# Kernel optimization log

Hardware: AMD Instinct MI355X
Metric: run time of the kernel (lower is better)

The kernel has to match this reference:

```python
import jax, jax.numpy as jnp
import numpy as np

N1, N2, D = 8192, 8192, 128

def setup_inputs() -> dict:
    key = jax.random.key(0)
    k1, k2, k3, k4 = jax.random.split(key, 4)
    X1 = jax.random.normal(k1, (N1, D), dtype=jnp.float32)
    X2 = jax.random.normal(k2, (N2, D), dtype=jnp.float32)
    task1 = jax.random.randint(k3, (N1,), 0, 2, dtype=jnp.int32)
    task2 = jax.random.randint(k4, (N2,), 0, 2, dtype=jnp.int32)
    # learned parameters (init values match module defaults: lengthscale=1, output_variance=1, b=0)
    log_l = jnp.zeros((D,), dtype=jnp.float32)          # log(1)
    log_theta_l = jnp.zeros((1,), dtype=jnp.float32)    # log(1)
    b = jnp.zeros((1,), dtype=jnp.float32)
    return {"X1": X1, "X2": X2, "log_l": log_l, "log_theta_l": log_theta_l,
            "b": b, "task1": task1, "task2": task2}

def reference(X1, X2, log_l, log_theta_l, b, task1, task2):
    l = jnp.exp(log_l)                      # (D,) ARD lengthscales
    A = X1 / l                              # (N1, D)
    B = X2 / l                              # (N2, D)
    # sum((a-b)^2) = |a|^2 + |b|^2 - 2 a.b  -> GEMM form, no (N1,N2,D) intermediate
    sq_dist = (jnp.sum(A * A, axis=1)[:, None]
               + jnp.sum(B * B, axis=1)[None, :]
               - 2.0 * (A @ B.T))
    sq_dist = jnp.maximum(sq_dist, 0.0)
    K_base = jnp.exp(log_theta_l[0]) * jnp.exp(-0.5 * sq_dist)   # (N1, N2)
    # lambda = clip(2/(1+exp(b)) - 1, 0, 1)
    lam = jnp.clip(2.0 / (1.0 + jnp.exp(b[0])) - 1.0, 0.0, 1.0)
    diff_task = task1[:, None] != task2[None, :]                 # (N1, N2) bool
    K = K_base * jnp.where(diff_task, lam, 1.0)
    return K
```

## Files before the change

kernel.cpp:

```cpp
#include <hip/hip_runtime.h>
#include <stdint.h>

typedef float f32x4 __attribute__((ext_vector_type(4)));
typedef int   i32x4 __attribute__((ext_vector_type(4)));
typedef __bf16 bf16x8 __attribute__((ext_vector_type(8)));

#define NN 8192
#define DDIM 128
#define RSTRIDE 80

#define OFF_AH 0
#define OFF_AL 10240
#define OFF_BH 20480
#define OFF_BL 30720
#define OFF_ILS 40960
#define OFF_N1  41472
#define OFF_N2  41984
#define LDS_TOT 42496

__device__ __forceinline__ uint32_t pk2(__bf16 a, __bf16 b) {
    return (uint32_t)__builtin_bit_cast(unsigned short, a)
         | ((uint32_t)__builtin_bit_cast(unsigned short, b) << 16);
}

__device__ __forceinline__ void split4(f32x4 x, uint2& hi, uint2& lo) {
    __bf16 h0 = (__bf16)x[0], h1 = (__bf16)x[1], h2 = (__bf16)x[2], h3 = (__bf16)x[3];
    hi.x = pk2(h0, h1); hi.y = pk2(h2, h3);
    __bf16 l0 = (__bf16)(x[0] - (float)h0);
    __bf16 l1 = (__bf16)(x[1] - (float)h1);
    __bf16 l2 = (__bf16)(x[2] - (float)h2);
    __bf16 l3 = (__bf16)(x[3] - (float)h3);
    lo.x = pk2(l0, l1); lo.y = pk2(l2, l3);
}

__device__ __forceinline__ void lds_barrier() {
    asm volatile("s_waitcnt lgkmcnt(0)" ::: "memory");
    __builtin_amdgcn_sched_barrier(0);
    __builtin_amdgcn_s_barrier();
    __builtin_amdgcn_sched_barrier(0);
}

__global__ __launch_bounds__(256, 3) void tgp_kernel(
    const float* __restrict__ X1, const float* __restrict__ X2,
    const float* __restrict__ log_l,
    const float* __restrict__ log_theta_l, const float* __restrict__ bparam,
    const int* __restrict__ task1, const int* __restrict__ task2,
    float* __restrict__ C)
{
    __shared__ __align__(16) char smem[LDS_TOT];
    float* const ils = (float*)(smem + OFF_ILS);
    float* const n1s = (float*)(smem + OFF_N1);
    float* const n2s = (float*)(smem + OFF_N2);

    const int t = threadIdx.x;
    const int lane = t & 63;
    const int wv = t >> 6;
    const int wr = wv >> 1, wc = wv & 1;
    const int lr = lane & 15, lg = lane >> 4;
    const int kq = t & 7;
    const int rg = t >> 3;

    int wg = blockIdx.x;
    int xcd = wg & 7;
    int r = wg >> 3;
    int su = r >> 6;
    int inner = r & 63;
    int tm = xcd * 8 + (inner >> 3);
    int tn = su * 8 + (inner & 7);

    const float* Ag = X1 + (size_t)tm * 128 * DDIM;
    const float* Bg = X2 + (size_t)tn * 128 * DDIM;

    if (t < 128) ils[t] = __expf(-log_l[t]);

    f32x4 aV[4], bV[4];
    #pragma unroll
    for (int e = 0; e < 4; ++e) {
        aV[e] = *(const f32x4*)(Ag + (size_t)(e * 32 + rg) * DDIM + kq * 4);
        bV[e] = *(const f32x4*)(Bg + (size_t)(e * 32 + rg) * DDIM + kq * 4);
    }
    __syncthreads();

    float nA[4] = {0.f, 0.f, 0.f, 0.f};
    float nB[4] = {0.f, 0.f, 0.f, 0.f};
    f32x4 acc[4][4];
    #pragma unroll
    for (int i = 0; i < 4; ++i)
        #pragma unroll
        for (int j = 0; j < 4; ++j) acc[i][j] = (f32x4){0.f, 0.f, 0.f, 0.f};

    for (int c = 0; c < 4; ++c) {
        f32x4 il4 = *(const f32x4*)(ils + c * 32 + kq * 4);
        #pragma unroll
        for (int e = 0; e < 4; ++e) {
            int rr = e * 32 + rg;
            f32x4 xa = aV[e] * il4;
            f32x4 xb = bV[e] * il4;
            nA[e] += xa[0]*xa[0] + xa[1]*xa[1] + xa[2]*xa[2] + xa[3]*xa[3];
            nB[e] += xb[0]*xb[0] + xb[1]*xb[1] + xb[2]*xb[2] + xb[3]*xb[3];
            uint2 hA, lA, hB, lB;
            split4(xa, hA, lA);
            split4(xb, hB, lB);
            int boff = rr * RSTRIDE + kq * 8;
            *(uint2*)(smem + OFF_AH + boff) = hA;
            *(uint2*)(smem + OFF_AL + boff) = lA;
            *(uint2*)(smem + OFF_BH + boff) = hB;
            *(uint2*)(smem + OFF_BL + boff) = lB;
        }
        if (c < 3) {
            #pragma unroll
            for (int e = 0; e < 4; ++e) {
                aV[e] = *(const f32x4*)(Ag + (size_t)(e * 32 + rg) * DDIM + (c + 1) * 32 + kq * 4);
                bV[e] = *(const f32x4*)(Bg + (size_t)(e * 32 + rg) * DDIM + (c + 1) * 32 + kq * 4);
            }
        }
        lds_barrier();

        {
            bf16x8 ah[4], bh[4], xf[4];
            #pragma unroll
            for (int mi = 0; mi < 4; ++mi) {
                int off = (wr * 64 + mi * 16 + lr) * RSTRIDE + lg * 16;
                ah[mi] = *(const bf16x8*)(smem + OFF_AH + off);
            }
            #pragma unroll
            for (int ni = 0; ni < 4; ++ni) {
                int off = (wc * 64 + ni * 16 + lr) * RSTRIDE + lg * 16;
                bh[ni] = *(const bf16x8*)(smem + OFF_BH + off);
            }
            #pragma unroll
            for (int mi = 0; mi < 4; ++mi)
                #pragma unroll
                for (int ni = 0; ni < 4; ++ni)
                    acc[mi][ni] = __builtin_amdgcn_mfma_f32_16x16x32_bf16(bh[ni], ah[mi], acc[mi][ni], 0, 0, 0);
            #pragma unroll
            for (int mi = 0; mi < 4; ++mi) {
                int off = (wr * 64 + mi * 16 + lr) * RSTRIDE + lg * 16;
                xf[mi] = *(const bf16x8*)(smem + OFF_AL + off);
            }
            #pragma unroll
            for (int mi = 0; mi < 4; ++mi)
                #pragma unroll
                for (int ni = 0; ni < 4; ++ni)
                    acc[mi][ni] = __builtin_amdgcn_mfma_f32_16x16x32_bf16(bh[ni], xf[mi], acc[mi][ni], 0, 0, 0);
            #pragma unroll
            for (int ni = 0; ni < 4; ++ni) {
                int off = (wc * 64 + ni * 16 + lr) * RSTRIDE + lg * 16;
                xf[ni] = *(const bf16x8*)(smem + OFF_BL + off);
            }
            #pragma unroll
            for (int mi = 0; mi < 4; ++mi)
                #pragma unroll
                for (int ni = 0; ni < 4; ++ni)
                    acc[mi][ni] = __builtin_amdgcn_mfma_f32_16x16x32_bf16(xf[ni], ah[mi], acc[mi][ni], 0, 0, 0);
        }
        lds_barrier();
    }

    #pragma unroll
    for (int e = 0; e < 4; ++e) {
        #pragma unroll
        for (int off = 1; off < 8; off <<= 1) {
            nA[e] += __shfl_xor(nA[e], off);
            nB[e] += __shfl_xor(nB[e], off);
        }
    }
    if ((t & 7) == 0) {
        #pragma unroll
        for (int e = 0; e < 4; ++e) {
            n1s[e * 32 + rg] = nA[e];
            n2s[e * 32 + rg] = nB[e];
        }
    }
    __syncthreads();

    float logt = log_theta_l[0];
    float bb = bparam[0];
    float lam = fminf(fmaxf(2.f / (1.f + __expf(bb)) - 1.f, 0.f), 1.f);
    int rbase = tm * 128, cbase = tn * 128;

    #pragma unroll
    for (int mi = 0; mi < 4; ++mi) {
        int rowl = wr * 64 + mi * 16 + lr;
        float n1v = n1s[rowl];
        int t1v = task1[rbase + rowl];
        #pragma unroll
        for (int ni = 0; ni < 4; ++ni) {
            int coll = wc * 64 + ni * 16 + lg * 4;
            f32x4 n2v = *(const f32x4*)(n2s + coll);
            i32x4 t2v = *(const i32x4*)(task2 + cbase + coll);
            f32x4 kv;
            #pragma unroll
            for (int rix = 0; rix < 4; ++rix) {
                float s = fmaxf(n1v + n2v[rix] - 2.f * acc[mi][ni][rix], 0.f);
                float k = __expf(fmaf(-0.5f, s, logt));
                kv[rix] = (t1v != t2v[rix]) ? k * lam : k;
            }
            *(f32x4*)(C + (size_t)(rbase + rowl) * NN + cbase + coll) = kv;
        }
    }
}

extern "C" void kernel_launch(void* const* d_in, const int* in_sizes, int n_in,
                              void* d_out, int out_size, void* d_ws, size_t ws_size,
                              hipStream_t stream)
{
    const float* X1 = (const float*)d_in[0];
    const float* X2 = (const float*)d_in[1];
    const float* log_l = (const float*)d_in[2];
    const float* log_theta = (const float*)d_in[3];
    const float* bp = (const float*)d_in[4];
    const int* t1 = (const int*)d_in[5];
    const int* t2 = (const int*)d_in[6];
    float* C = (float*)d_out;
    (void)d_ws; (void)ws_size; (void)in_sizes; (void)n_in; (void)out_size;

    tgp_kernel<<<4096, 256, 0, stream>>>(X1, X2, log_l, log_theta, bp, t1, t2, C);
}
```

Baseline: 98.62 us.

## Use 512-thread blocks with 64-wide K chunks and an 8-wave output split

The block grows from 4 to 8 waves. Each wave now computes a 64x32 sub-tile instead of 64x64. The K dimension is staged in two 64-wide chunks rather than four 32-wide chunks, with a larger LDS row stride, so there are fewer barriers and the trailing barrier is gone. The register prefetch of the next chunk is removed, so global loads are no longer overlapped with MFMA work. LDS per block roughly doubles, which may limit how many blocks fit on a CU, in exchange for more waves per block to hide the latency of the output stores.

```diff
diff --git a/kernel.cpp b/kernel.cpp
--- a/kernel.cpp
+++ b/kernel.cpp
@@ -7,16 +7,16 @@
 
 #define NN 8192
 #define DDIM 128
-#define RSTRIDE 80
+#define RSTRIDE 144
 
 #define OFF_AH 0
-#define OFF_AL 10240
-#define OFF_BH 20480
-#define OFF_BL 30720
-#define OFF_ILS 40960
-#define OFF_N1  41472
-#define OFF_N2  41984
-#define LDS_TOT 42496
+#define OFF_AL 18432
+#define OFF_BH 36864
+#define OFF_BL 55296
+#define OFF_ILS 73728
+#define OFF_N1  74240
+#define OFF_N2  74752
+#define LDS_TOT 75264
 
 __device__ __forceinline__ uint32_t pk2(__bf16 a, __bf16 b) {
     return (uint32_t)__builtin_bit_cast(unsigned short, a)
@@ -40,7 +40,7 @@
     __builtin_amdgcn_sched_barrier(0);
 }
 
-__global__ __launch_bounds__(256, 3) void tgp_kernel(
+__global__ __launch_bounds__(512, 4) void tgp_kernel(
     const float* __restrict__ X1, const float* __restrict__ X2,
     const float* __restrict__ log_l,
     const float* __restrict__ log_theta_l, const float* __restrict__ bparam,
@@ -55,10 +55,10 @@
     const int t = threadIdx.x;
     const int lane = t & 63;
     const int wv = t >> 6;
-    const int wr = wv >> 1, wc = wv & 1;
+    const int wr = wv >> 2, wc = wv & 3;
     const int lr = lane & 15, lg = lane >> 4;
-    const int kq = t & 7;
-    const int rg = t >> 3;
+    const int kq = t & 15;
+    const int rg = t >> 4;
 
     int wg = blockIdx.x;
     int xcd = wg & 7;
@@ -72,100 +72,92 @@
     const float* Bg = X2 + (size_t)tn * 128 * DDIM;
 
     if (t < 128) ils[t] = __expf(-log_l[t]);
-
-    f32x4 aV[4], bV[4];
-    #pragma unroll
-    for (int e = 0; e < 4; ++e) {
-        aV[e] = *(const f32x4*)(Ag + (size_t)(e * 32 + rg) * DDIM + kq * 4);
-        bV[e] = *(const f32x4*)(Bg + (size_t)(e * 32 + rg) * DDIM + kq * 4);
-    }
     __syncthreads();
 
     float nA[4] = {0.f, 0.f, 0.f, 0.f};
     float nB[4] = {0.f, 0.f, 0.f, 0.f};
-    f32x4 acc[4][4];
+    f32x4 acc[4][2];
     #pragma unroll
     for (int i = 0; i < 4; ++i)
         #pragma unroll
-        for (int j = 0; j < 4; ++j) acc[i][j] = (f32x4){0.f, 0.f, 0.f, 0.f};
-
-    for (int c = 0; c < 4; ++c) {
-        f32x4 il4 = *(const f32x4*)(ils + c * 32 + kq * 4);
-        #pragma unroll
-        for (int e = 0; e < 4; ++e) {
-            int rr = e * 32 + rg;
-            f32x4 xa = aV[e] * il4;
-            f32x4 xb = bV[e] * il4;
-            nA[e] += xa[0]*xa[0] + xa[1]*xa[1] + xa[2]*xa[2] + xa[3]*xa[3];
-            nB[e] += xb[0]*xb[0] + xb[1]*xb[1] + xb[2]*xb[2] + xb[3]*xb[3];
-            uint2 hA, lA, hB, lB;
-            split4(xa, hA, lA);
-            split4(xb, hB, lB);
-            int boff = rr * RSTRIDE + kq * 8;
-            *(uint2*)(smem + OFF_AH + boff) = hA;
-            *(uint2*)(smem + OFF_AL + boff) = lA;
-            *(uint2*)(smem + OFF_BH + boff) = hB;
-            *(uint2*)(smem + OFF_BL + boff) = lB;
-        }
-        if (c < 3) {
+        for (int j = 0; j < 2; ++j) acc[i][j] = (f32x4){0.f, 0.f, 0.f, 0.f};
+
+    #pragma unroll
+    for (int c = 0; c < 2; ++c) {
+        {
+            f32x4 il4 = *(const f32x4*)(ils + c * 64 + kq * 4);
             #pragma unroll
             for (int e = 0; e < 4; ++e) {
-                aV[e] = *(const f32x4*)(Ag + (size_t)(e * 32 + rg) * DDIM + (c + 1) * 32 + kq * 4);
-                bV[e] = *(const f32x4*)(Bg + (size_t)(e * 32 + rg) * DDIM + (c + 1) * 32 + kq * 4);
+                int row = e * 32 + rg;
+                f32x4 xa = *(const f32x4*)(Ag + (size_t)row * DDIM + c * 64 + kq * 4);
+                f32x4 xb = *(const f32x4*)(Bg + (size_t)row * DDIM + c * 64 + kq * 4);
+                xa *= il4; xb *= il4;
+                nA[e] += xa[0]*xa[0] + xa[1]*xa[1] + xa[2]*xa[2] + xa[3]*xa[3];
+                nB[e] += xb[0]*xb[0] + xb[1]*xb[1] + xb[2]*xb[2] + xb[3]*xb[3];
+                uint2 hA, lA, hB, lB;
+                split4(xa, hA, lA);
+                split4(xb, hB, lB);
+                int boff = row * RSTRIDE + kq * 8;
+                *(uint2*)(smem + OFF_AH + boff) = hA;
+                *(uint2*)(smem + OFF_AL + boff) = lA;
+                *(uint2*)(smem + OFF_BH + boff) = hB;
+                *(uint2*)(smem + OFF_BL + boff) = lB;
             }
         }
         lds_barrier();
 
-        {
-            bf16x8 ah[4], bh[4], xf[4];
+        #pragma unroll
+        for (int ks = 0; ks < 2; ++ks) {
+            int kb = ks * 64;
+            bf16x8 ah[4], bx[2], xf[4];
             #pragma unroll
             for (int mi = 0; mi < 4; ++mi) {
-                int off = (wr * 64 + mi * 16 + lr) * RSTRIDE + lg * 16;
+                int off = (wr * 64 + mi * 16 + lr) * RSTRIDE + kb + lg * 16;
                 ah[mi] = *(const bf16x8*)(smem + OFF_AH + off);
             }
             #pragma unroll
-            for (int ni = 0; ni < 4; ++ni) {
-                int off = (wc * 64 + ni * 16 + lr) * RSTRIDE + lg * 16;
-                bh[ni] = *(const bf16x8*)(smem + OFF_BH + off);
+            for (int ni = 0; ni < 2; ++ni) {
+                int off = (wc * 32 + ni * 16 + lr) * RSTRIDE + kb + lg * 16;
+                bx[ni] = *(const bf16x8*)(smem + OFF_BH + off);
             }
             #pragma unroll
             for (int mi = 0; mi < 4; ++mi)
                 #pragma unroll
-                for (int ni = 0; ni < 4; ++ni)
-                    acc[mi][ni] = __builtin_amdgcn_mfma_f32_16x16x32_bf16(bh[ni], ah[mi], acc[mi][ni], 0, 0, 0);
+                for (int ni = 0; ni < 2; ++ni)
+                    acc[mi][ni] = __builtin_amdgcn_mfma_f32_16x16x32_bf16(bx[ni], ah[mi], acc[mi][ni], 0, 0, 0);
             #pragma unroll
             for (int mi = 0; mi < 4; ++mi) {
-                int off = (wr * 64 + mi * 16 + lr) * RSTRIDE + lg * 16;
+                int off = (wr * 64 + mi * 16 + lr) * RSTRIDE + kb + lg * 16;
                 xf[mi] = *(const bf16x8*)(smem + OFF_AL + off);
             }
             #pragma unroll
             for (int mi = 0; mi < 4; ++mi)
                 #pragma unroll
-                for (int ni = 0; ni < 4; ++ni)
-                    acc[mi][ni] = __builtin_amdgcn_mfma_f32_16x16x32_bf16(bh[ni], xf[mi], acc[mi][ni], 0, 0, 0);
-            #pragma unroll
-            for (int ni = 0; ni < 4; ++ni) {
-                int off = (wc * 64 + ni * 16 + lr) * RSTRIDE + lg * 16;
-                xf[ni] = *(const bf16x8*)(smem + OFF_BL + off);
+                for (int ni = 0; ni < 2; ++ni)
+                    acc[mi][ni] = __builtin_amdgcn_mfma_f32_16x16x32_bf16(bx[ni], xf[mi], acc[mi][ni], 0, 0, 0);
+            #pragma unroll
+            for (int ni = 0; ni < 2; ++ni) {
+                int off = (wc * 32 + ni * 16 + lr) * RSTRIDE + kb + lg * 16;
+                bx[ni] = *(const bf16x8*)(smem + OFF_BL + off);
             }
             #pragma unroll
             for (int mi = 0; mi < 4; ++mi)
                 #pragma unroll
-                for (int ni = 0; ni < 4; ++ni)
-                    acc[mi][ni] = __builtin_amdgcn_mfma_f32_16x16x32_bf16(xf[ni], ah[mi], acc[mi][ni], 0, 0, 0);
-        }
-        lds_barrier();
+                for (int ni = 0; ni < 2; ++ni)
+                    acc[mi][ni] = __builtin_amdgcn_mfma_f32_16x16x32_bf16(bx[ni], ah[mi], acc[mi][ni], 0, 0, 0);
+        }
+        if (c == 0) lds_barrier();
     }
 
     #pragma unroll
     for (int e = 0; e < 4; ++e) {
         #pragma unroll
-        for (int off = 1; off < 8; off <<= 1) {
+        for (int off = 1; off < 16; off <<= 1) {
             nA[e] += __shfl_xor(nA[e], off);
             nB[e] += __shfl_xor(nB[e], off);
         }
     }
-    if ((t & 7) == 0) {
+    if (kq == 0) {
         #pragma unroll
         for (int e = 0; e < 4; ++e) {
             n1s[e * 32 + rg] = nA[e];
@@ -185,8 +177,8 @@
         float n1v = n1s[rowl];
         int t1v = task1[rbase + rowl];
         #pragma unroll
-        for (int ni = 0; ni < 4; ++ni) {
-            int coll = wc * 64 + ni * 16 + lg * 4;
+        for (int ni = 0; ni < 2; ++ni) {
+            int coll = wc * 32 + ni * 16 + lg * 4;
             f32x4 n2v = *(const f32x4*)(n2s + coll);
             i32x4 t2v = *(const i32x4*)(task2 + cbase + coll);
             f32x4 kv;
@@ -215,5 +207,5 @@
     float* C = (float*)d_out;
     (void)d_ws; (void)ws_size; (void)in_sizes; (void)n_in; (void)out_size;
 
-    tgp_kernel<<<4096, 256, 0, stream>>>(X1, X2, log_l, log_theta, bp, t1, t2, C);
-}
+    tgp_kernel<<<4096, 512, 0, stream>>>(X1, X2, log_l, log_theta, bp, t1, t2, C);
+}
```

New measurement: 103.6 us. 1.05x slower.

## Double-buffer LDS tiles to overlap bf16 split with MFMA compute

Applied to the files above, without the earlier changes.

Restructures the K loop into a manually unrolled, double-buffered pipeline. The split and LDS write of the next 32-column chunk now run right after the MFMAs on the current buffer, which cuts one barrier per chunk. It also shrinks the LDS row stride from 80 to 72 bytes, and raises wave priority during the MFMA phase with s_setprio. LDS use nearly doubles, so launch bounds drop from 3 to 2 blocks per CU, lowering occupancy in exchange for overlap.

```diff
diff --git a/kernel.cpp b/kernel.cpp
--- a/kernel.cpp
+++ b/kernel.cpp
@@ -7,16 +7,18 @@
 
 #define NN 8192
 #define DDIM 128
-#define RSTRIDE 80
+#define RSTRIDE 72
+#define TILE_B 9216
+#define BUF_B  36864
 
 #define OFF_AH 0
-#define OFF_AL 10240
-#define OFF_BH 20480
-#define OFF_BL 30720
-#define OFF_ILS 40960
-#define OFF_N1  41472
-#define OFF_N2  41984
-#define LDS_TOT 42496
+#define OFF_AL 9216
+#define OFF_BH 18432
+#define OFF_BL 27648
+#define OFF_ILS 73728
+#define OFF_N1  74240
+#define OFF_N2  74752
+#define LDS_TOT 75264
 
 __device__ __forceinline__ uint32_t pk2(__bf16 a, __bf16 b) {
     return (uint32_t)__builtin_bit_cast(unsigned short, a)
@@ -40,7 +42,7 @@
     __builtin_amdgcn_sched_barrier(0);
 }
 
-__global__ __launch_bounds__(256, 3) void tgp_kernel(
+__global__ __launch_bounds__(256, 2) void tgp_kernel(
     const float* __restrict__ X1, const float* __restrict__ X2,
     const float* __restrict__ log_l,
     const float* __restrict__ log_theta_l, const float* __restrict__ bparam,
@@ -71,91 +73,102 @@
     const float* Ag = X1 + (size_t)tm * 128 * DDIM;
     const float* Bg = X2 + (size_t)tn * 128 * DDIM;
 
-    if (t < 128) ils[t] = __expf(-log_l[t]);
-
     f32x4 aV[4], bV[4];
-    #pragma unroll
-    for (int e = 0; e < 4; ++e) {
-        aV[e] = *(const f32x4*)(Ag + (size_t)(e * 32 + rg) * DDIM + kq * 4);
-        bV[e] = *(const f32x4*)(Bg + (size_t)(e * 32 + rg) * DDIM + kq * 4);
-    }
-    __syncthreads();
+    #define LOADC(c) do {                                                        \
+        _Pragma("unroll")                                                        \
+        for (int e = 0; e < 4; ++e) {                                            \
+            aV[e] = *(const f32x4*)(Ag + (size_t)(e * 32 + rg) * DDIM + (c) * 32 + kq * 4); \
+            bV[e] = *(const f32x4*)(Bg + (size_t)(e * 32 + rg) * DDIM + (c) * 32 + kq * 4); \
+        }                                                                        \
+    } while (0)
 
     float nA[4] = {0.f, 0.f, 0.f, 0.f};
     float nB[4] = {0.f, 0.f, 0.f, 0.f};
+
+    #define SPLITW(c, bb) do {                                                   \
+        f32x4 il4 = *(const f32x4*)(ils + (c) * 32 + kq * 4);                    \
+        char* base = smem + (bb) * BUF_B;                                        \
+        _Pragma("unroll")                                                        \
+        for (int e = 0; e < 4; ++e) {                                            \
+            int row = e * 32 + rg;                                               \
+            f32x4 xa = aV[e] * il4;                                              \
+            f32x4 xb = bV[e] * il4;                                              \
+            nA[e] += xa[0]*xa[0] + xa[1]*xa[1] + xa[2]*xa[2] + xa[3]*xa[3];      \
+            nB[e] += xb[0]*xb[0] + xb[1]*xb[1] + xb[2]*xb[2] + xb[3]*xb[3];      \
+            uint2 hA, lA, hB, lB;                                                \
+            split4(xa, hA, lA);                                                  \
+            split4(xb, hB, lB);                                                  \
+            int boff = row * RSTRIDE + kq * 8;                                   \
+            *(uint2*)(base + OFF_AH + boff) = hA;                                \
+            *(uint2*)(base + OFF_AL + boff) = lA;                                \
+            *(uint2*)(base + OFF_BH + boff) = hB;                                \
+            *(uint2*)(base + OFF_BL + boff) = lB;                                \
+        }                                                                        \
+    } while (0)
+
     f32x4 acc[4][4];
     #pragma unroll
     for (int i = 0; i < 4; ++i)
         #pragma unroll
         for (int j = 0; j < 4; ++j) acc[i][j] = (f32x4){0.f, 0.f, 0.f, 0.f};
 
-    for (int c = 0; c < 4; ++c) {
-        f32x4 il4 = *(const f32x4*)(ils + c * 32 + kq * 4);
-        #pragma unroll
-        for (int e = 0; e < 4; ++e) {
-            int rr = e * 32 + rg;
-            f32x4 xa = aV[e] * il4;
-            f32x4 xb = bV[e] * il4;
-            nA[e] += xa[0]*xa[0] + xa[1]*xa[1] + xa[2]*xa[2] + xa[3]*xa[3];
-            nB[e] += xb[0]*xb[0] + xb[1]*xb[1] + xb[2]*xb[2] + xb[3]*xb[3];
-            uint2 hA, lA, hB, lB;
-            split4(xa, hA, lA);
-            split4(xb, hB, lB);
-            int boff = rr * RSTRIDE + kq * 8;
-            *(uint2*)(smem + OFF_AH + boff) = hA;
-            *(uint2*)(smem + OFF_AL + boff) = lA;
-            *(uint2*)(smem + OFF_BH + boff) = hB;
-            *(uint2*)(smem + OFF_BL + boff) = lB;
-        }
-        if (c < 3) {
-            #pragma unroll
-            for (int e = 0; e < 4; ++e) {
-                aV[e] = *(const f32x4*)(Ag + (size_t)(e * 32 + rg) * DDIM + (c + 1) * 32 + kq * 4);
-                bV[e] = *(const f32x4*)(Bg + (size_t)(e * 32 + rg) * DDIM + (c + 1) * 32 + kq * 4);
-            }
-        }
-        lds_barrier();
-
-        {
-            bf16x8 ah[4], bh[4], xf[4];
-            #pragma unroll
-            for (int mi = 0; mi < 4; ++mi) {
-                int off = (wr * 64 + mi * 16 + lr) * RSTRIDE + lg * 16;
-                ah[mi] = *(const bf16x8*)(smem + OFF_AH + off);
-            }
-            #pragma unroll
-            for (int ni = 0; ni < 4; ++ni) {
-                int off = (wc * 64 + ni * 16 + lr) * RSTRIDE + lg * 16;
-                bh[ni] = *(const bf16x8*)(smem + OFF_BH + off);
-            }
-            #pragma unroll
-            for (int mi = 0; mi < 4; ++mi)
-                #pragma unroll
-                for (int ni = 0; ni < 4; ++ni)
-                    acc[mi][ni] = __builtin_amdgcn_mfma_f32_16x16x32_bf16(bh[ni], ah[mi], acc[mi][ni], 0, 0, 0);
-            #pragma unroll
-            for (int mi = 0; mi < 4; ++mi) {
-                int off = (wr * 64 + mi * 16 + lr) * RSTRIDE + lg * 16;
-                xf[mi] = *(const bf16x8*)(smem + OFF_AL + off);
-            }
-            #pragma unroll
-            for (int mi = 0; mi < 4; ++mi)
-                #pragma unroll
-                for (int ni = 0; ni < 4; ++ni)
-                    acc[mi][ni] = __builtin_amdgcn_mfma_f32_16x16x32_bf16(bh[ni], xf[mi], acc[mi][ni], 0, 0, 0);
-            #pragma unroll
-            for (int ni = 0; ni < 4; ++ni) {
-                int off = (wc * 64 + ni * 16 + lr) * RSTRIDE + lg * 16;
-                xf[ni] = *(const bf16x8*)(smem + OFF_BL + off);
-            }
-            #pragma unroll
-            for (int mi = 0; mi < 4; ++mi)
-                #pragma unroll
-                for (int ni = 0; ni < 4; ++ni)
-                    acc[mi][ni] = __builtin_amdgcn_mfma_f32_16x16x32_bf16(xf[ni], ah[mi], acc[mi][ni], 0, 0, 0);
-        }
-        lds_barrier();
-    }
+    #define FRAGMM(bb) do {                                                      \
+        const char* base = smem + (bb) * BUF_B;                                  \
+        bf16x8 ah[4], bh[4], xf[4];                                              \
+        __builtin_amdgcn_s_setprio(1);                                           \
+        _Pragma("unroll")                                                        \
+        for (int mi = 0; mi < 4; ++mi) {                                         \
+            int off = (wr * 64 + mi * 16 + lr) * RSTRIDE + lg * 16;              \
+            ah[mi] = *(const bf16x8*)(base + OFF_AH + off);                      \
+        }                                                                        \
+        _Pragma("unroll")                                                        \
+        for (int ni = 0; ni < 4; ++ni) {                                         \
+            int off = (wc * 64 + ni * 16 + lr) * RSTRIDE + lg * 16;              \
+            bh[ni] = *(const bf16x8*)(base + OFF_BH + off);                      \
+        }                                                                        \
+        _Pragma("unroll")                                                        \
+        for (int mi = 0; mi < 4; ++mi)                                           \
+            _Pragma("unroll")                                                    \
+            for (int ni = 0; ni < 4; ++ni)                                       \
+                acc[mi][ni] = __builtin_amdgcn_mfma_f32_16x16x32_bf16(bh[ni], ah[mi], acc[mi][ni], 0, 0, 0); \
+        _Pragma("unroll")                                                        \
+        for (int mi = 0; mi < 4; ++mi) {                                         \
+            int off = (wr * 64 + mi * 16 + lr) * RSTRIDE + lg * 16;              \
+            xf[mi] = *(const bf16x8*)(base + OFF_AL + off);                      \
+        }                                                                        \
+        _Pragma("unroll")                                                        \
+        for (int mi = 0; mi < 4; ++mi)                                           \
+            _Pragma("unroll")                                                    \
+            for (int ni = 0; ni < 4; ++ni)                                       \
+                acc[mi][ni] = __builtin_amdgcn_mfma_f32_16x16x32_bf16(bh[ni], xf[mi], acc[mi][ni], 0, 0, 0); \
+        _Pragma("unroll")                                                        \
+        for (int ni = 0; ni < 4; ++ni) {                                         \
+            int off = (wc * 64 + ni * 16 + lr) * RSTRIDE + lg * 16;              \
+            xf[ni] = *(const bf16x8*)(base + OFF_BL + off);                      \
+        }                                                                        \
+        _Pragma("unroll")                                                        \
+        for (int mi = 0; mi < 4; ++mi)                                           \
+            _Pragma("unroll")                                                    \
+            for (int ni = 0; ni < 4; ++ni)                                       \
+                acc[mi][ni] = __builtin_amdgcn_mfma_f32_16x16x32_bf16(xf[ni], ah[mi], acc[mi][ni], 0, 0, 0); \
+        __builtin_amdgcn_s_setprio(0);                                           \
+    } while (0)
+
+    LOADC(0);
+    if (t < 128) ils[t] = __expf(-log_l[t]);
+    __syncthreads();
+    SPLITW(0, 0);
+    LOADC(1);
+    lds_barrier();
+
+    FRAGMM(0); SPLITW(1, 1); LOADC(2); lds_barrier();
+    FRAGMM(1); SPLITW(2, 0); LOADC(3); lds_barrier();
+    FRAGMM(0); SPLITW(3, 1);           lds_barrier();
+    FRAGMM(1);
+
+    #undef LOADC
+    #undef SPLITW
+    #undef FRAGMM
 
     #pragma unroll
     for (int e = 0; e < 4; ++e) {
@@ -165,7 +178,7 @@
             nB[e] += __shfl_xor(nB[e], off);
         }
     }
-    if ((t & 7) == 0) {
+    if (kq == 0) {
         #pragma unroll
         for (int e = 0; e < 4; ++e) {
             n1s[e * 32 + rg] = nA[e];
```

After: 179.6 us. +82.1%, slower.

## Make each workgroup compute four column tiles, overlapping next-tile loads with epilogue

Applied to the files above, without the earlier changes.

Each workgroup now loops over four consecutive 128-column tiles of X2 for one row tile, so the grid drops from 4096 to 1024 blocks. Row norms and task ids for A are computed once and kept in registers, and the first chunk of the next B tile is prefetched during the last K-chunk of the current tile. The aim is to cut per-block launch overhead and amortise the A-side setup, at the cost of redoing the A split and LDS writes per tile and fewer blocks for load balance across CUs.

```diff
diff --git a/kernel.cpp b/kernel.cpp
--- a/kernel.cpp
+++ b/kernel.cpp
@@ -63,13 +63,13 @@
     int wg = blockIdx.x;
     int xcd = wg & 7;
     int r = wg >> 3;
-    int su = r >> 6;
-    int inner = r & 63;
-    int tm = xcd * 8 + (inner >> 3);
-    int tn = su * 8 + (inner & 7);
+    int su = r >> 4;
+    int inner = r & 15;
+    int tm = xcd * 8 + (inner >> 1);
+    int tnb = su * 8 + (inner & 1) * 4;
 
     const float* Ag = X1 + (size_t)tm * 128 * DDIM;
-    const float* Bg = X2 + (size_t)tn * 128 * DDIM;
+    const float* Bg = X2 + (size_t)tnb * 128 * DDIM;
 
     if (t < 128) ils[t] = __expf(-log_l[t]);
 
@@ -82,122 +82,138 @@
     __syncthreads();
 
     float nA[4] = {0.f, 0.f, 0.f, 0.f};
-    float nB[4] = {0.f, 0.f, 0.f, 0.f};
-    f32x4 acc[4][4];
-    #pragma unroll
-    for (int i = 0; i < 4; ++i)
-        #pragma unroll
-        for (int j = 0; j < 4; ++j) acc[i][j] = (f32x4){0.f, 0.f, 0.f, 0.f};
-
-    for (int c = 0; c < 4; ++c) {
-        f32x4 il4 = *(const f32x4*)(ils + c * 32 + kq * 4);
-        #pragma unroll
-        for (int e = 0; e < 4; ++e) {
-            int rr = e * 32 + rg;
-            f32x4 xa = aV[e] * il4;
-            f32x4 xb = bV[e] * il4;
-            nA[e] += xa[0]*xa[0] + xa[1]*xa[1] + xa[2]*xa[2] + xa[3]*xa[3];
-            nB[e] += xb[0]*xb[0] + xb[1]*xb[1] + xb[2]*xb[2] + xb[3]*xb[3];
-            uint2 hA, lA, hB, lB;
-            split4(xa, hA, lA);
-            split4(xb, hB, lB);
-            int boff = rr * RSTRIDE + kq * 8;
-            *(uint2*)(smem + OFF_AH + boff) = hA;
-            *(uint2*)(smem + OFF_AL + boff) = lA;
-            *(uint2*)(smem + OFF_BH + boff) = hB;
-            *(uint2*)(smem + OFF_BL + boff) = lB;
-        }
-        if (c < 3) {
-            #pragma unroll
-            for (int e = 0; e < 4; ++e) {
-                aV[e] = *(const f32x4*)(Ag + (size_t)(e * 32 + rg) * DDIM + (c + 1) * 32 + kq * 4);
-                bV[e] = *(const f32x4*)(Bg + (size_t)(e * 32 + rg) * DDIM + (c + 1) * 32 + kq * 4);
-            }
-        }
-        lds_barrier();
-
-        {
-            bf16x8 ah[4], bh[4], xf[4];
-            #pragma unroll
-            for (int mi = 0; mi < 4; ++mi) {
-                int off = (wr * 64 + mi * 16 + lr) * RSTRIDE + lg * 16;
-                ah[mi] = *(const bf16x8*)(smem + OFF_AH + off);
-            }
-            #pragma unroll
-            for (int ni = 0; ni < 4; ++ni) {
-                int off = (wc * 64 + ni * 16 + lr) * RSTRIDE + lg * 16;
-                bh[ni] = *(const bf16x8*)(smem + OFF_BH + off);
-            }
-            #pragma unroll
-            for (int mi = 0; mi < 4; ++mi)
-                #pragma unroll
-                for (int ni = 0; ni < 4; ++ni)
-                    acc[mi][ni] = __builtin_amdgcn_mfma_f32_16x16x32_bf16(bh[ni], ah[mi], acc[mi][ni], 0, 0, 0);
-            #pragma unroll
-            for (int mi = 0; mi < 4; ++mi) {
-                int off = (wr * 64 + mi * 16 + lr) * RSTRIDE + lg * 16;
-                xf[mi] = *(const bf16x8*)(smem + OFF_AL + off);
-            }
-            #pragma unroll
-            for (int mi = 0; mi < 4; ++mi)
-                #pragma unroll
-                for (int ni = 0; ni < 4; ++ni)
-                    acc[mi][ni] = __builtin_amdgcn_mfma_f32_16x16x32_bf16(bh[ni], xf[mi], acc[mi][ni], 0, 0, 0);
-            #pragma unroll
-            for (int ni = 0; ni < 4; ++ni) {
-                int off = (wc * 64 + ni * 16 + lr) * RSTRIDE + lg * 16;
-                xf[ni] = *(const bf16x8*)(smem + OFF_BL + off);
-            }
-            #pragma unroll
-            for (int mi = 0; mi < 4; ++mi)
-                #pragma unroll
-                for (int ni = 0; ni < 4; ++ni)
-                    acc[mi][ni] = __builtin_amdgcn_mfma_f32_16x16x32_bf16(xf[ni], ah[mi], acc[mi][ni], 0, 0, 0);
-        }
-        lds_barrier();
-    }
-
-    #pragma unroll
-    for (int e = 0; e < 4; ++e) {
-        #pragma unroll
-        for (int off = 1; off < 8; off <<= 1) {
-            nA[e] += __shfl_xor(nA[e], off);
-            nB[e] += __shfl_xor(nB[e], off);
-        }
-    }
-    if ((t & 7) == 0) {
-        #pragma unroll
-        for (int e = 0; e < 4; ++e) {
-            n1s[e * 32 + rg] = nA[e];
-            n2s[e * 32 + rg] = nB[e];
-        }
-    }
-    __syncthreads();
-
+    float n1r[4]; int t1r[4];
     float logt = log_theta_l[0];
     float bb = bparam[0];
     float lam = fminf(fmaxf(2.f / (1.f + __expf(bb)) - 1.f, 0.f), 1.f);
-    int rbase = tm * 128, cbase = tn * 128;
-
-    #pragma unroll
-    for (int mi = 0; mi < 4; ++mi) {
-        int rowl = wr * 64 + mi * 16 + lr;
-        float n1v = n1s[rowl];
-        int t1v = task1[rbase + rowl];
+    int rbase = tm * 128;
+
+    for (int j = 0; j < 4; ++j) {
+        f32x4 acc[4][4];
         #pragma unroll
-        for (int ni = 0; ni < 4; ++ni) {
-            int coll = wc * 64 + ni * 16 + lg * 4;
-            f32x4 n2v = *(const f32x4*)(n2s + coll);
-            i32x4 t2v = *(const i32x4*)(task2 + cbase + coll);
-            f32x4 kv;
+        for (int i = 0; i < 4; ++i)
             #pragma unroll
-            for (int rix = 0; rix < 4; ++rix) {
-                float s = fmaxf(n1v + n2v[rix] - 2.f * acc[mi][ni][rix], 0.f);
-                float k = __expf(fmaf(-0.5f, s, logt));
-                kv[rix] = (t1v != t2v[rix]) ? k * lam : k;
-            }
-            *(f32x4*)(C + (size_t)(rbase + rowl) * NN + cbase + coll) = kv;
+            for (int k = 0; k < 4; ++k) acc[i][k] = (f32x4){0.f, 0.f, 0.f, 0.f};
+        float nB[4] = {0.f, 0.f, 0.f, 0.f};
+
+        for (int c = 0; c < 4; ++c) {
+            {
+                f32x4 il4 = *(const f32x4*)(ils + c * 32 + kq * 4);
+                #pragma unroll
+                for (int e = 0; e < 4; ++e) {
+                    int row = e * 32 + rg;
+                    f32x4 xa = aV[e] * il4;
+                    f32x4 xb = bV[e] * il4;
+                    if (j == 0)
+                        nA[e] += xa[0]*xa[0] + xa[1]*xa[1] + xa[2]*xa[2] + xa[3]*xa[3];
+                    nB[e] += xb[0]*xb[0] + xb[1]*xb[1] + xb[2]*xb[2] + xb[3]*xb[3];
+                    uint2 hA, lA, hB, lB;
+                    split4(xa, hA, lA);
+                    split4(xb, hB, lB);
+                    int boff = row * RSTRIDE + kq * 8;
+                    *(uint2*)(smem + OFF_AH + boff) = hA;
+                    *(uint2*)(smem + OFF_AL + boff) = lA;
+                    *(uint2*)(smem + OFF_BH + boff) = hB;
+                    *(uint2*)(smem + OFF_BL + boff) = lB;
+                }
+            }
+            if (c < 3) {
+                #pragma unroll
+                for (int e = 0; e < 4; ++e) {
+                    aV[e] = *(const f32x4*)(Ag + (size_t)(e * 32 + rg) * DDIM + (c + 1) * 32 + kq * 4);
+                    bV[e] = *(const f32x4*)(Bg + (size_t)(e * 32 + rg) * DDIM + (c + 1) * 32 + kq * 4);
+                }
+            } else if (j < 3) {
+                #pragma unroll
+                for (int e = 0; e < 4; ++e) {
+                    aV[e] = *(const f32x4*)(Ag + (size_t)(e * 32 + rg) * DDIM + kq * 4);
+                    bV[e] = *(const f32x4*)(Bg + 16384 + (size_t)(e * 32 + rg) * DDIM + kq * 4);
+                }
+            }
+            if (c == 3) {
+                #pragma unroll
+                for (int e = 0; e < 4; ++e) {
+                    #pragma unroll
+                    for (int off = 1; off < 8; off <<= 1) {
+                        nB[e] += __shfl_xor(nB[e], off);
+                        if (j == 0) nA[e] += __shfl_xor(nA[e], off);
+                    }
+                }
+                if (kq == 0) {
+                    #pragma unroll
+                    for (int e = 0; e < 4; ++e) {
+                        n2s[e * 32 + rg] = nB[e];
+                        if (j == 0) n1s[e * 32 + rg] = nA[e];
+                    }
+                }
+            }
+            lds_barrier();
+
+            {
+                bf16x8 ah[4], bh[4], xf[4];
+                #pragma unroll
+                for (int mi = 0; mi < 4; ++mi) {
+                    int off = (wr * 64 + mi * 16 + lr) * RSTRIDE + lg * 16;
+                    ah[mi] = *(const bf16x8*)(smem + OFF_AH + off);
+                }
+                #pragma unroll
+                for (int ni = 0; ni < 4; ++ni) {
+                    int off = (wc * 64 + ni * 16 + lr) * RSTRIDE + lg * 16;
+                    bh[ni] = *(const bf16x8*)(smem + OFF_BH + off);
+                }
+                #pragma unroll
+                for (int mi = 0; mi < 4; ++mi)
+                    #pragma unroll
+                    for (int ni = 0; ni < 4; ++ni)
+                        acc[mi][ni] = __builtin_amdgcn_mfma_f32_16x16x32_bf16(bh[ni], ah[mi], acc[mi][ni], 0, 0, 0);
+                #pragma unroll
+                for (int mi = 0; mi < 4; ++mi) {
+                    int off = (wr * 64 + mi * 16 + lr) * RSTRIDE + lg * 16;
+                    xf[mi] = *(const bf16x8*)(smem + OFF_AL + off);
+                }
+                #pragma unroll
+                for (int mi = 0; mi < 4; ++mi)
+                    #pragma unroll
+                    for (int ni = 0; ni < 4; ++ni)
+                        acc[mi][ni] = __builtin_amdgcn_mfma_f32_16x16x32_bf16(bh[ni], xf[mi], acc[mi][ni], 0, 0, 0);
+                #pragma unroll
+                for (int ni = 0; ni < 4; ++ni) {
+                    int off = (wc * 64 + ni * 16 + lr) * RSTRIDE + lg * 16;
+                    xf[ni] = *(const bf16x8*)(smem + OFF_BL + off);
+                }
+                #pragma unroll
+                for (int mi = 0; mi < 4; ++mi)
+                    #pragma unroll
+                    for (int ni = 0; ni < 4; ++ni)
+                        acc[mi][ni] = __builtin_amdgcn_mfma_f32_16x16x32_bf16(xf[ni], ah[mi], acc[mi][ni], 0, 0, 0);
+            }
+            lds_barrier();
         }
+
+        int cbase = (tnb + j) * 128;
+        #pragma unroll
+        for (int mi = 0; mi < 4; ++mi) {
+            int rowl = wr * 64 + mi * 16 + lr;
+            if (j == 0) {
+                n1r[mi] = n1s[rowl];
+                t1r[mi] = task1[rbase + rowl];
+            }
+            #pragma unroll
+            for (int ni = 0; ni < 4; ++ni) {
+                int coll = wc * 64 + ni * 16 + lg * 4;
+                f32x4 n2v = *(const f32x4*)(n2s + coll);
+                i32x4 t2v = *(const i32x4*)(task2 + cbase + coll);
+                f32x4 kv;
+                #pragma unroll
+                for (int rix = 0; rix < 4; ++rix) {
+                    float s = fmaxf(n1r[mi] + n2v[rix] - 2.f * acc[mi][ni][rix], 0.f);
+                    float k = __expf(fmaf(-0.5f, s, logt));
+                    kv[rix] = (t1r[mi] != t2v[rix]) ? k * lam : k;
+                }
+                *(f32x4*)(C + (size_t)(rbase + rowl) * NN + cbase + coll) = kv;
+            }
+        }
+        Bg += 128 * DDIM;
     }
 }
 
@@ -215,5 +231,5 @@
     float* C = (float*)d_out;
     (void)d_ws; (void)ws_size; (void)in_sizes; (void)n_in; (void)out_size;
 
-    tgp_kernel<<<4096, 256, 0, stream>>>(X1, X2, log_l, log_theta, bp, t1, t2, C);
-}
+    tgp_kernel<<<1024, 256, 0, stream>>>(X1, X2, log_l, log_theta, bp, t1, t2, C);
+}
```

After: 140.7 us. 1.43x slower.
